# Performance work log

Hardware: AMD Instinct MI355X
Metric: run time of the kernel (lower is better)

## Reference

```python
import jax, jax.numpy as jnp
import numpy as np

V_MIN = -10.0
V_MAX = 10.0
NUM_ATOMS = 51
ATOM_DELTA = (V_MAX - V_MIN) / (NUM_ATOMS - 1)
BS = 1_000_000


def setup_inputs() -> dict:
    key = jax.random.key(0)
    k1, k2 = jax.random.split(key)
    reward = jax.random.normal(k1, (BS,), dtype=jnp.float32) * 3.0
    probs = jax.random.uniform(k2, (BS, NUM_ATOMS), dtype=jnp.float32)
    atom_values = (V_MIN + ATOM_DELTA * jnp.arange(NUM_ATOMS)).astype(jnp.float32)
    return {"reward": reward, "probs": probs, "atom_values": atom_values}


def reference(reward, probs, atom_values):
    # Categorical (C51) Bellman projection, expressed as a scatter-add
    # instead of the original's dense [bs, A, A] projection matrix + bmm.
    bs, A = probs.shape
    # shifted & clamped atom support: [bs, A]
    new_vals = jnp.clip(atom_values[None, :] + reward[:, None], V_MIN, V_MAX)
    idx = (new_vals - V_MIN) / ATOM_DELTA           # fractional atom index
    lower = jnp.floor(idx)
    upper = jnp.ceil(idx)
    same = lower == upper                           # idx landed exactly on an atom
    l_coef = jnp.where(same, 1.0, upper - idx)      # original sets 1.0 when l == u
    u_coef = idx - lower                            # 0 when same
    li = lower.astype(jnp.int32)
    ui = upper.astype(jnp.int32)
    rows = jnp.broadcast_to(jnp.arange(bs)[:, None], (bs, A))
    out = jnp.zeros_like(probs)
    out = out.at[rows, li].add(l_coef * probs)
    out = out.at[rows, ui].add(u_coef * probs)
    return out
```

## Files before the change

### kernel.cpp

```cpp
#include <hip/hip_runtime.h>

#define NA 51
#define TPB 128
#define WROWS 64
#define KCLAMP 52

typedef float v4u __attribute__((ext_vector_type(4), aligned(4)));
typedef float v2u __attribute__((ext_vector_type(2), aligned(4)));
typedef float v4a __attribute__((ext_vector_type(4), aligned(16)));

__global__ __launch_bounds__(TPB, 3) void c51_bellman_kernel(
    const float* __restrict__ reward,
    const float* __restrict__ probs,
    float* __restrict__ out,
    int bs)
{
    __shared__ __align__(16) float lds[TPB * NA];
    const int tid   = threadIdx.x;
    const int lane  = tid & 63;
    const int wv    = tid >> 6;
    const int wrow0 = blockIdx.x * TPB + wv * WROWS;
    const int r     = wrow0 + lane;
    const bool edge = (blockIdx.x == 0) | (blockIdx.x == (int)gridDim.x - 1);

    float* const wlds = lds + wv * (WROWS * NA);
    const int nrows_w = min(WROWS, max(0, bs - wrow0));

    if (lane < nrows_w) {
        const float s  = reward[r] * 2.5f;
        const float kf = floorf(s);
        const float f  = s - kf;
        int k = (int)kf;
        k = min(max(k, -KCLAMP), KCLAMP);
        const float* rp = probs + (size_t)r * NA;

        float row[NA];
        #pragma unroll
        for (int c = 0; c < 12; ++c) *(v4u*)&row[4 * c] = *(const v4u*)&rp[4 * c];
        *(v2u*)&row[48] = *(const v2u*)&rp[48];
        row[50] = rp[50];

        float w[52];
        if (!edge) {
            const float* wb = rp - k - 1;
            #pragma unroll
            for (int c = 0; c < 13; ++c) *(v4u*)&w[4 * c] = *(const v4u*)&wb[4 * c];
        } else {
            #pragma unroll
            for (int m = 0; m < 52; ++m)
                w[m] = rp[min(max(m - k - 1, 0), NA - 1)];
        }

        float m_lo = 0.0f, m_hi = 0.0f;
        #pragma unroll
        for (int j = 0; j < NA; ++j) {
            const float t = (float)j + s;
            if (t < 0.0f)  m_lo += row[j];
            if (t > 50.0f) m_hi += row[j];
        }

        float* wp = wlds + lane * NA;
        const float w1 = 1.0f - f;
        float prev = ((unsigned)(-k - 1) <= 50u) ? w[0] : 0.0f;
        #pragma unroll
        for (int i = 0; i < NA; ++i) {
            const float cur = ((unsigned)(i - k) <= 50u) ? w[i + 1] : 0.0f;
            float o;
            if (i == 0)           o = w1 * cur + m_lo;
            else if (i == NA - 1) o = ((f == 0.0f) ? cur : f * prev) + m_hi;
            else                  o = w1 * cur + f * prev;
            wp[i] = o;
            prev = cur;
        }
    }

    const int nelem = nrows_w * NA;
    const int n4    = nelem >> 2;
    const v4a* l4 = (const v4a*)wlds;
    v4a* o4 = (v4a*)(out + (size_t)wrow0 * NA);
    for (int e = lane; e < n4; e += 64) o4[e] = l4[e];
    for (int e = (n4 << 2) + lane; e < nelem; e += 64)
        out[(size_t)wrow0 * NA + e] = wlds[e];
}

extern "C" void kernel_launch(void* const* d_in, const int* in_sizes, int n_in,
                              void* d_out, int out_size, void* d_ws, size_t ws_size,
                              hipStream_t stream) {
    const float* reward = (const float*)d_in[0];
    const float* probs  = (const float*)d_in[1];
    float* out = (float*)d_out;
    const int bs = in_sizes[0];

    const int blocks = (bs + TPB - 1) / TPB;
    c51_bellman_kernel<<<blocks, TPB, 0, stream>>>(reward, probs, out, bs);
}
```

Baseline: 347.3 us.

## Split each row across four lanes with shuffle-reduced edge masses

Each C51 row is now handled by four lanes, each owning 13 atoms, instead of one thread per row. Edge probability masses are combined with xor shuffles, and each wave stages 16 rows in LDS before a coalesced store. Blocks grow to 256 threads covering 64 rows, with a higher occupancy hint. The aim is to cut per-thread register arrays, raise occupancy and make global loads across neighbouring lanes more contiguous. The cost is redundant shifted-window loads and shuffle overhead.

```diff
diff --git a/kernel.cpp b/kernel.cpp
--- a/kernel.cpp
+++ b/kernel.cpp
@@ -1,32 +1,36 @@
 #include <hip/hip_runtime.h>
 
 #define NA 51
-#define TPB 128
-#define WROWS 64
+#define TPB 256
+#define RPW 16
+#define RPB 64
 #define KCLAMP 52
 
 typedef float v4u __attribute__((ext_vector_type(4), aligned(4)));
 typedef float v2u __attribute__((ext_vector_type(2), aligned(4)));
 typedef float v4a __attribute__((ext_vector_type(4), aligned(16)));
 
-__global__ __launch_bounds__(TPB, 3) void c51_bellman_kernel(
+__global__ __launch_bounds__(TPB, 8) void c51_bellman_kernel(
     const float* __restrict__ reward,
     const float* __restrict__ probs,
     float* __restrict__ out,
     int bs)
 {
-    __shared__ __align__(16) float lds[TPB * NA];
-    const int tid   = threadIdx.x;
-    const int lane  = tid & 63;
-    const int wv    = tid >> 6;
-    const int wrow0 = blockIdx.x * TPB + wv * WROWS;
-    const int r     = wrow0 + lane;
+    __shared__ __align__(16) float lds[4][RPW * NA];
+    const int tid  = threadIdx.x;
+    const int lane = tid & 63;
+    const int wv   = tid >> 6;
+    const int q    = lane & 3;
+    const int lr   = lane >> 2;
+    const int wrow0 = blockIdx.x * RPB + wv * RPW;
+    const int r     = wrow0 + lr;
     const bool edge = (blockIdx.x == 0) | (blockIdx.x == (int)gridDim.x - 1);
 
-    float* const wlds = lds + wv * (WROWS * NA);
-    const int nrows_w = min(WROWS, max(0, bs - wrow0));
+    float* const wlds = lds[wv];
+    const int a0    = 13 * q;
+    const int count = (q < 3) ? 13 : 12;
 
-    if (lane < nrows_w) {
+    if (r < bs) {
         const float s  = reward[r] * 2.5f;
         const float kf = floorf(s);
         const float f  = s - kf;
@@ -34,47 +38,52 @@
         k = min(max(k, -KCLAMP), KCLAMP);
         const float* rp = probs + (size_t)r * NA;
 
-        float row[NA];
-        #pragma unroll
-        for (int c = 0; c < 12; ++c) *(v4u*)&row[4 * c] = *(const v4u*)&rp[4 * c];
-        *(v2u*)&row[48] = *(const v2u*)&rp[48];
-        row[50] = rp[50];
+        float row[13];
+        *(v4u*)&row[0] = *(const v4u*)&rp[a0];
+        *(v4u*)&row[4] = *(const v4u*)&rp[a0 + 4];
+        *(v4u*)&row[8] = *(const v4u*)&rp[a0 + 8];
+        row[12] = (q < 3) ? rp[a0 + 12] : 0.0f;
 
-        float w[52];
+        float w[14];
         if (!edge) {
-            const float* wb = rp - k - 1;
-            #pragma unroll
-            for (int c = 0; c < 13; ++c) *(v4u*)&w[4 * c] = *(const v4u*)&wb[4 * c];
+            const float* wb = rp + a0 - k - 1;
+            *(v4u*)&w[0]  = *(const v4u*)&wb[0];
+            *(v4u*)&w[4]  = *(const v4u*)&wb[4];
+            *(v4u*)&w[8]  = *(const v4u*)&wb[8];
+            *(v2u*)&w[12] = *(const v2u*)&wb[12];
         } else {
             #pragma unroll
-            for (int m = 0; m < 52; ++m)
-                w[m] = rp[min(max(m - k - 1, 0), NA - 1)];
+            for (int m = 0; m < 14; ++m)
+                w[m] = rp[min(max(a0 + m - k - 1, 0), NA - 1)];
         }
 
         float m_lo = 0.0f, m_hi = 0.0f;
         #pragma unroll
-        for (int j = 0; j < NA; ++j) {
-            const float t = (float)j + s;
-            if (t < 0.0f)  m_lo += row[j];
-            if (t > 50.0f) m_hi += row[j];
+        for (int c = 0; c < 13; ++c) {
+            const float t = (float)(a0 + c) + s;
+            if (t < 0.0f)  m_lo += row[c];
+            if (t > 50.0f) m_hi += row[c];
         }
+        m_lo += __shfl_xor(m_lo, 1, 64); m_lo += __shfl_xor(m_lo, 2, 64);
+        m_hi += __shfl_xor(m_hi, 1, 64); m_hi += __shfl_xor(m_hi, 2, 64);
 
-        float* wp = wlds + lane * NA;
         const float w1 = 1.0f - f;
-        float prev = ((unsigned)(-k - 1) <= 50u) ? w[0] : 0.0f;
+        float* wp = wlds + lr * NA + a0;
         #pragma unroll
-        for (int i = 0; i < NA; ++i) {
-            const float cur = ((unsigned)(i - k) <= 50u) ? w[i + 1] : 0.0f;
+        for (int c = 0; c < 13; ++c) {
+            const int i = a0 + c;
+            const float pl = ((unsigned)(i - k - 1) <= 50u) ? w[c]     : 0.0f;
+            const float cu = ((unsigned)(i - k)     <= 50u) ? w[c + 1] : 0.0f;
             float o;
-            if (i == 0)           o = w1 * cur + m_lo;
-            else if (i == NA - 1) o = ((f == 0.0f) ? cur : f * prev) + m_hi;
-            else                  o = w1 * cur + f * prev;
-            wp[i] = o;
-            prev = cur;
+            if (i == 0)           o = w1 * cu + m_lo;
+            else if (i == NA - 1) o = ((f == 0.0f) ? cu : f * pl) + m_hi;
+            else                  o = w1 * cu + f * pl;
+            if (c < count) wp[c] = o;
         }
     }
 
-    const int nelem = nrows_w * NA;
+    const int nrw   = min(RPW, max(0, bs - wrow0));
+    const int nelem = nrw * NA;
     const int n4    = nelem >> 2;
     const v4a* l4 = (const v4a*)wlds;
     v4a* o4 = (v4a*)(out + (size_t)wrow0 * NA);
@@ -91,6 +100,6 @@
     float* out = (float*)d_out;
     const int bs = in_sizes[0];
 
-    const int blocks = (bs + TPB - 1) / TPB;
+    const int blocks = (bs + RPB - 1) / RPB;
     c51_bellman_kernel<<<blocks, TPB, 0, stream>>>(reward, probs, out, bs);
 }
```

Measured after the change: 341.2 us. No clear change (-1.8%).
